# Kernel optimization log

Hardware: AMD Instinct MI355X
Metric: run time of the kernel (lower is better)

Reference implementation:

```python
import jax, jax.numpy as jnp
import numpy as np

K = 5  # kernel_size


def _unfold(x, k):
    """Torch F.unfold equivalent: [B,C,H,W] -> [B,C,k*k,H,W].
    Patch index is row-major over the kxk window (dy*k+dx), matching
    F.unfold's channel-major / window-row-major layout after view(B,C,k*k,H,W)."""
    p = k // 2
    B, C, H, W = x.shape
    xp = jnp.pad(x, ((0, 0), (0, 0), (p, p), (p, p)))
    patches = [xp[:, :, dy:dy + H, dx:dx + W] for dy in range(k) for dx in range(k)]
    return jnp.stack(patches, axis=2)


def _conv2d(x, w, b, pad):
    y = jax.lax.conv_general_dilated(
        x, w, window_strides=(1, 1), padding=[(pad, pad), (pad, pad)],
        dimension_numbers=("NCHW", "OIHW", "NCHW"))
    return y + b[None, :, None, None]


def setup_inputs() -> dict:
    key = jax.random.key(0)
    k0, k1, k2 = jax.random.split(key, 3)
    B, H, W = 2, 1024, 1024
    flow = jax.random.normal(k0, (B, 2, H, W), jnp.float32)
    # kernel_gen params: Conv2d(3,32,3,pad=1) -> ReLU -> Conv2d(32,50,1)
    w1 = jax.random.normal(k1, (32, 3, 3, 3), jnp.float32) * 0.1
    b1 = jnp.zeros((32,), jnp.float32)
    w2 = jax.random.normal(k2, (K * K * 2, 32, 1, 1), jnp.float32) * 0.1
    b2 = jnp.zeros((K * K * 2,), jnp.float32)
    return {"flow": flow, "w1": w1, "b1": b1, "w2": w2, "b2": b2}


def reference(flow, w1, b1, w2, b2):
    B, _, H, W = flow.shape
    patches = _unfold(flow, K)                       # [B,2,25,H,W]
    # torch .var(dim=2) defaults to unbiased (ddof=1)
    var = jnp.var(patches, axis=2, ddof=1)           # [B,2,H,W]
    consistency = jnp.exp(-jnp.sqrt(jnp.sum(var * var, axis=1, keepdims=True)))  # [B,1,H,W]
    guidance = jnp.concatenate([flow, consistency], axis=1)  # [B,3,H,W]
    h = jax.nn.relu(_conv2d(guidance, w1, b1, pad=1))        # [B,32,H,W]
    kernels = _conv2d(h, w2, b2, pad=0).reshape(B, 2, K * K, H, W)
    refined = jnp.sum(kernels * patches, axis=2)             # [B,2,H,W]
    return refined
```

## Files before the change

kernel.cpp:

```cpp
#include <hip/hip_runtime.h>
#include <math.h>

#define KSZ 5
#define TS 16
#define HALO 3
#define FW (TS + 2*HALO)
#define FWP (FW + 1)
#define CW (TS + 2)
#define CWP (CW + 1)
#define SF_C (FW*FWP)
#define SC_BASE (2*SF_C)

typedef __attribute__((ext_vector_type(8))) short short8_t;
typedef __attribute__((ext_vector_type(4))) float float4_t;
typedef __attribute__((ext_vector_type(2))) unsigned int uint2_t;

static __device__ __forceinline__ unsigned short f2bf(float f) {
    union { float f; unsigned int u; } v; v.f = f;
    return (unsigned short)((v.u + 0x7FFFu + ((v.u >> 16) & 1u)) >> 16);
}
static __device__ __forceinline__ unsigned int pk2t(float a, float b) {
    union { float f; unsigned int u; } ua, ub; ua.f = a; ub.f = b;
    return __builtin_amdgcn_perm(ub.u, ua.u, 0x07060302u);
}

static __device__ __forceinline__ void slot_decode(int n, int& c, int& sel, int& idx, bool& valid) {
    int g4c = (n >> 2) & 3;
    c = g4c >> 1; sel = g4c & 1;
    idx = ((n >> 4) << 2) + (n & 3);
    valid = sel ? (idx < 10) : (idx < 15);
}

__global__ __launch_bounds__(256)
void pack_kernel(const float* __restrict__ w1, const float* __restrict__ b1,
                 const float* __restrict__ w2, const float* __restrict__ b2,
                 unsigned short* __restrict__ wp, float* __restrict__ bp)
{
    const int tid = threadIdx.x;
    for (int i = tid; i < 6*64*8; i += 256) {
        int f = i >> 9, l = (i >> 3) & 63, j = i & 7;
        int m = l & 15, k = ((l >> 4) << 3) + j;
        float v;
        if (f < 2) { int row = f*16 + m; v = (k < 27) ? w1[row*27 + k] : 0.f; }
        else {
            int n = (f - 2)*16 + m;
            int c, sel, idx; bool valid;
            slot_decode(n, c, sel, idx, valid);
            int jj = sel*15 + idx;
            v = valid ? w2[(c*25 + jj)*32 + k] : 0.f;
        }
        wp[i] = f2bf(v);
    }
    for (int i = tid; i < 6*64*4; i += 256) {
        int f = i >> 8, l = (i >> 2) & 63, r = i & 3, g4 = l >> 4;
        float v;
        if (f < 2) v = b1[f*16 + g4*4 + r];
        else {
            int n = (f - 2)*16 + g4*4 + r;
            int c, sel, idx; bool valid;
            slot_decode(n, c, sel, idx, valid);
            v = valid ? b2[c*25 + sel*15 + idx] : 0.f;
        }
        bp[i] = v;
    }
}

__global__ __launch_bounds__(256)
void refine_kernel(const float* __restrict__ flow,
                   const unsigned short* __restrict__ wp,
                   const float* __restrict__ bp,
                   float* __restrict__ out, int H, int W)
{
    __shared__ float smf[SC_BASE + CW*CWP];
    __shared__ __align__(16) char dyn[6400];

    const int tid = threadIdx.x;
    const int x0 = blockIdx.x * TS;
    const int y0 = blockIdx.y * TS;
    const int b  = blockIdx.z;

    const int lane = tid & 63;
    const int wave = tid >> 6;
    const int col  = lane & 15;
    const int g4   = lane >> 4;
    const int key  = col >> 2;

    short8_t w1A[2], w2A[4];
    float4_t cb1[2], cb2[4];
    #pragma unroll
    for (int nt = 0; nt < 2; ++nt) {
        w1A[nt] = *(const short8_t*)&wp[(nt*64 + lane)*8];
        cb1[nt] = *(const float4_t*)&bp[(nt*64 + lane)*4];
    }
    #pragma unroll
    for (int nt = 0; nt < 4; ++nt) {
        w2A[nt] = *(const short8_t*)&wp[((2+nt)*64 + lane)*8];
        cb2[nt] = *(const float4_t*)&bp[((2+nt)*64 + lane)*4];
    }

    for (int c = 0; c < 2; ++c) {
        const float* src = flow + ((size_t)(b*2+c) * H) * W;
        for (int i = tid; i < FW*FW; i += 256) {
            int ly = i / FW, lx = i - ly*FW;
            int gy = y0 - HALO + ly, gx = x0 - HALO + lx;
            float v = 0.f;
            if (gy >= 0 && gy < H && gx >= 0 && gx < W) v = src[(size_t)gy*W + gx];
            smf[c*SF_C + ly*FWP + lx] = v;
        }
    }
    __syncthreads();

    {
        float4_t* rs = (float4_t*)dyn;
        for (int i = tid; i < FW*CW; i += 256) {
            int y = i / CW, x = i - y*CW;
            const float* r0 = &smf[y*FWP + x];
            const float* r1 = &smf[SF_C + y*FWP + x];
            float s0 = 0.f, q0 = 0.f, s1 = 0.f, q1 = 0.f;
            #pragma unroll
            for (int dx = 0; dx < KSZ; ++dx) {
                float a = r0[dx]; s0 += a; q0 = fmaf(a, a, q0);
                float c = r1[dx]; s1 += c; q1 = fmaf(c, c, q1);
            }
            rs[i] = (float4_t){s0, q0, s1, q1};
        }
    }
    __syncthreads();

    for (int i = tid; i < CW*CW; i += 256) {
        int py = i / CW, px = i - py*CW;
        int gy = y0 - 1 + py, gx = x0 - 1 + px;
        float cons = 0.f;
        if (gy >= 0 && gy < H && gx >= 0 && gx < W) {
            const float4_t* rp = (const float4_t*)dyn + py*CW + px;
            float4_t acc = rp[0];
            #pragma unroll
            for (int dy = 1; dy < KSZ; ++dy) acc += rp[dy*CW];
            float v0 = (acc.y - acc.x*acc.x*(1.f/25.f)) * (1.f/24.f);
            float v1 = (acc.w - acc.z*acc.z*(1.f/25.f)) * (1.f/24.f);
            cons = __expf(-sqrtf(v0*v0 + v1*v1));
        }
        smf[SC_BASE + py*CWP + px] = cons;
    }
    __syncthreads();

    unsigned short* hb = (unsigned short*)dyn;

    int goff[8], gpitch[8];
    #pragma unroll
    for (int j = 0; j < 8; ++j) {
        int ch = g4*8 + j;
        int chc = (ch < 27) ? ch : 0;
        int c = chc / 9, rem = chc - 9*c;
        int ky = rem / 3, kx = rem - 3*ky;
        if (c < 2) { goff[j] = c*SF_C + (2+ky)*FWP + (2+kx) + col; gpitch[j] = FWP; }
        else       { goff[j] = SC_BASE + ky*CWP + kx + col;        gpitch[j] = CWP; }
        goff[j] += wave*4 * gpitch[j];
    }

    const int sel = g4 & 1, pc = g4 >> 1;
    int pb = pc*SF_C + sel*(3*FWP) + FWP + 1 + col + (wave*4)*FWP;

    const int hrow = (wave*16 + col) * 64;
    const int hw0 = hrow + (((0*2 + (g4 >> 1)) ^ key) << 4) + ((g4 & 1) << 3);
    const int hw1 = hrow + (((1*2 + (g4 >> 1)) ^ key) << 4) + ((g4 & 1) << 3);
    const int hro = hrow + ((g4 ^ key) << 4);

    #pragma unroll
    for (int mt = 0; mt < 4; ++mt) {
        const int ty = wave*4 + mt;

        unsigned int gd[4];
        #pragma unroll
        for (int t = 0; t < 4; ++t)
            gd[t] = pk2t(smf[goff[2*t]], smf[goff[2*t+1]]);
        #pragma unroll
        for (int j = 0; j < 8; ++j) goff[j] += gpitch[j];
        union { unsigned int u[4]; short8_t s; } gu;
        gu.u[0] = gd[0]; gu.u[1] = gd[1]; gu.u[2] = gd[2]; gu.u[3] = gd[3];
        short8_t gB = gu.s;

        float4_t h0 = __builtin_amdgcn_mfma_f32_16x16x32_bf16(w1A[0], gB, cb1[0], 0, 0, 0);
        float4_t h1 = __builtin_amdgcn_mfma_f32_16x16x32_bf16(w1A[1], gB, cb1[1], 0, 0, 0);

        {
            uint2_t d0, d1;
            d0.x = pk2t(fmaxf(h0[0],0.f), fmaxf(h0[1],0.f));
            d0.y = pk2t(fmaxf(h0[2],0.f), fmaxf(h0[3],0.f));
            d1.x = pk2t(fmaxf(h1[0],0.f), fmaxf(h1[1],0.f));
            d1.y = pk2t(fmaxf(h1[2],0.f), fmaxf(h1[3],0.f));
            *(uint2_t*)((char*)hb + hw0) = d0;
            *(uint2_t*)((char*)hb + hw1) = d1;
        }
        short8_t hf = *(const short8_t*)((char*)hb + hro);

        float4_t ka[4];
        #pragma unroll
        for (int nt = 0; nt < 4; ++nt)
            ka[nt] = __builtin_amdgcn_mfma_f32_16x16x32_bf16(w2A[nt], hf, cb2[nt], 0, 0, 0);

        float s = 0.f;
        #pragma unroll
        for (int idx = 0; idx < 16; ++idx) {
            float pv = smf[pb + (idx/5)*FWP + (idx%5)];
            s = fmaf(ka[idx >> 2][idx & 3], pv, s);
        }
        pb += FWP;

        s += __shfl_xor(s, 16);

        if ((g4 & 1) == 0) {
            int y = y0 + ty, x = x0 + col;
            out[((size_t)(b*2 + pc) * H + y) * W + x] = s;
        }
    }
}

extern "C" void kernel_launch(void* const* d_in, const int* in_sizes, int n_in,
                              void* d_out, int out_size, void* d_ws, size_t ws_size,
                              hipStream_t stream) {
    const float* flow = (const float*)d_in[0];
    const float* w1   = (const float*)d_in[1];
    const float* b1   = (const float*)d_in[2];
    const float* w2   = (const float*)d_in[3];
    const float* b2   = (const float*)d_in[4];
    float* out = (float*)d_out;

    unsigned short* wp = (unsigned short*)d_ws;
    float* bp = (float*)((char*)d_ws + 8192);

    const int H = 1024, W = 1024;
    const int B = in_sizes[0] / (2 * H * W);

    pack_kernel<<<1, 256, 0, stream>>>(w1, b1, w2, b2, wp, bp);
    dim3 grid(W / TS, H / TS, B);
    refine_kernel<<<grid, dim3(256), 0, stream>>>(flow, wp, bp, out, H, W);
}
```

Before: 130.9 us.

## Permute conv1 K-slots for uniform LDS gathers and reuse patch rows in registers

The conv1 weight packing reorders the 27 input taps into K-slots, and the consistency map now uses the same pitch as the flow tiles. Together these let each lane gather its 8 bf16 operands from one base pointer plus constant offsets instead of 8 separately computed addresses. The 5-wide row-sum stage computes two outputs per thread with a sliding update, so fewer LDS reads are needed. In the main loop the 15 patch values are kept in registers and shifted by one row per iteration, so only 5 new LDS loads are issued each step. The cost is more register pressure and more complex index logic, and the sliding sums may round slightly differently.

```diff
diff --git a/kernel.cpp b/kernel.cpp
--- a/kernel.cpp
+++ b/kernel.cpp
@@ -7,9 +7,9 @@
 #define FW (TS + 2*HALO)
 #define FWP (FW + 1)
 #define CW (TS + 2)
-#define CWP (CW + 1)
 #define SF_C (FW*FWP)
 #define SC_BASE (2*SF_C)
+#define SMF_TOT (SC_BASE + 18*FWP)
 
 typedef __attribute__((ext_vector_type(8))) short short8_t;
 typedef __attribute__((ext_vector_type(4))) float float4_t;
@@ -29,6 +29,15 @@
     c = g4c >> 1; sel = g4c & 1;
     idx = ((n >> 4) << 2) + (n & 3);
     valid = sel ? (idx < 10) : (idx < 15);
+}
+
+static __device__ __forceinline__ int kperm(int s) {
+    int sg = s >> 3, sj = s & 7;
+    if (sg < 3) return sg*9 + sj;
+    if (sj == 1) return 8;
+    if (sj == 2) return 17;
+    if (sj == 4) return 26;
+    return -1;
 }
 
 __global__ __launch_bounds__(256)
@@ -39,15 +48,16 @@
     const int tid = threadIdx.x;
     for (int i = tid; i < 6*64*8; i += 256) {
         int f = i >> 9, l = (i >> 3) & 63, j = i & 7;
-        int m = l & 15, k = ((l >> 4) << 3) + j;
+        int m = l & 15, s = ((l >> 4) << 3) + j;
         float v;
-        if (f < 2) { int row = f*16 + m; v = (k < 27) ? w1[row*27 + k] : 0.f; }
-        else {
+        if (f < 2) {
+            int k = kperm(s);
+            v = (k >= 0) ? w1[(f*16 + m)*27 + k] : 0.f;
+        } else {
             int n = (f - 2)*16 + m;
             int c, sel, idx; bool valid;
             slot_decode(n, c, sel, idx, valid);
-            int jj = sel*15 + idx;
-            v = valid ? w2[(c*25 + jj)*32 + k] : 0.f;
+            v = valid ? w2[(c*25 + sel*15 + idx)*32 + s] : 0.f;
         }
         wp[i] = f2bf(v);
     }
@@ -71,7 +81,7 @@
                    const float* __restrict__ bp,
                    float* __restrict__ out, int H, int W)
 {
-    __shared__ float smf[SC_BASE + CW*CWP];
+    __shared__ float smf[SMF_TOT];
     __shared__ __align__(16) char dyn[6400];
 
     const int tid = threadIdx.x;
@@ -112,17 +122,22 @@
 
     {
         float4_t* rs = (float4_t*)dyn;
-        for (int i = tid; i < FW*CW; i += 256) {
-            int y = i / CW, x = i - y*CW;
-            const float* r0 = &smf[y*FWP + x];
-            const float* r1 = &smf[SF_C + y*FWP + x];
-            float s0 = 0.f, q0 = 0.f, s1 = 0.f, q1 = 0.f;
-            #pragma unroll
-            for (int dx = 0; dx < KSZ; ++dx) {
-                float a = r0[dx]; s0 += a; q0 = fmaf(a, a, q0);
-                float c = r1[dx]; s1 += c; q1 = fmaf(c, c, q1);
-            }
-            rs[i] = (float4_t){s0, q0, s1, q1};
+        if (tid < FW*(CW/2)) {
+            int y = tid / (CW/2), xp = (tid - y*(CW/2)) * 2;
+            const float* r0 = &smf[y*FWP + xp];
+            const float* r1 = &smf[SF_C + y*FWP + xp];
+            float a0=r0[0], a1=r0[1], a2=r0[2], a3=r0[3], a4=r0[4], a5=r0[5];
+            float c0=r1[0], c1=r1[1], c2=r1[2], c3=r1[3], c4=r1[4], c5=r1[5];
+            float sA = ((a0+a1)+(a2+a3))+a4;
+            float qA = fmaf(a4,a4, fmaf(a3,a3, fmaf(a2,a2, fmaf(a1,a1, a0*a0))));
+            float sB = ((c0+c1)+(c2+c3))+c4;
+            float qB = fmaf(c4,c4, fmaf(c3,c3, fmaf(c2,c2, fmaf(c1,c1, c0*c0))));
+            float sA1 = sA + a5 - a0;
+            float qA1 = fmaf(-a0, a0, fmaf(a5, a5, qA));
+            float sB1 = sB + c5 - c0;
+            float qB1 = fmaf(-c0, c0, fmaf(c5, c5, qB));
+            rs[y*CW + xp]     = (float4_t){sA,  qA,  sB,  qB };
+            rs[y*CW + xp + 1] = (float4_t){sA1, qA1, sB1, qB1};
         }
     }
     __syncthreads();
@@ -140,26 +155,29 @@
             float v1 = (acc.w - acc.z*acc.z*(1.f/25.f)) * (1.f/24.f);
             cons = __expf(-sqrtf(v0*v0 + v1*v1));
         }
-        smf[SC_BASE + py*CWP + px] = cons;
+        smf[SC_BASE + py*FWP + px] = cons;
     }
     __syncthreads();
 
     unsigned short* hb = (unsigned short*)dyn;
 
-    int goff[8], gpitch[8];
-    #pragma unroll
-    for (int j = 0; j < 8; ++j) {
-        int ch = g4*8 + j;
-        int chc = (ch < 27) ? ch : 0;
-        int c = chc / 9, rem = chc - 9*c;
-        int ky = rem / 3, kx = rem - 3*ky;
-        if (c < 2) { goff[j] = c*SF_C + (2+ky)*FWP + (2+kx) + col; gpitch[j] = FWP; }
-        else       { goff[j] = SC_BASE + ky*CWP + kx + col;        gpitch[j] = CWP; }
-        goff[j] += wave*4 * gpitch[j];
+    int gb0, gb1, gb2, gb3;
+    {
+        int ty0 = wave*4;
+        int p0 = 0*SF_C + (ty0 + 2)*FWP + (col + 2);
+        int p1 = 1*SF_C + (ty0 + 2)*FWP + (col + 2);
+        int p2 = SC_BASE + ty0*FWP + col;
+        if (g4 == 0)      { gb0 = gb1 = gb2 = gb3 = p0; }
+        else if (g4 == 1) { gb0 = gb1 = gb2 = gb3 = p1; }
+        else if (g4 == 2) { gb0 = gb1 = gb2 = gb3 = p2; }
+        else { gb0 = p0 + 47; gb1 = p1 + 46; gb2 = p2 + 24; gb3 = p0; }
     }
 
     const int sel = g4 & 1, pc = g4 >> 1;
     int pb = pc*SF_C + sel*(3*FWP) + FWP + 1 + col + (wave*4)*FWP;
+    float pv[15];
+    #pragma unroll
+    for (int i = 0; i < 15; ++i) pv[i] = smf[pb + (i/5)*FWP + (i%5)];
 
     const int hrow = (wave*16 + col) * 64;
     const int hw0 = hrow + (((0*2 + (g4 >> 1)) ^ key) << 4) + ((g4 & 1) << 3);
@@ -170,15 +188,15 @@
     for (int mt = 0; mt < 4; ++mt) {
         const int ty = wave*4 + mt;
 
-        unsigned int gd[4];
-        #pragma unroll
-        for (int t = 0; t < 4; ++t)
-            gd[t] = pk2t(smf[goff[2*t]], smf[goff[2*t+1]]);
-        #pragma unroll
-        for (int j = 0; j < 8; ++j) goff[j] += gpitch[j];
+        float ga = smf[gb0 + 0],  gbv = smf[gb0 + 1];
+        float gc = smf[gb1 + 2],  gd  = smf[gb1 + 23];
+        float ge = smf[gb2 + 24], gf  = smf[gb2 + 25];
+        float gg = smf[gb3 + 46], gh  = smf[gb3 + 47];
         union { unsigned int u[4]; short8_t s; } gu;
-        gu.u[0] = gd[0]; gu.u[1] = gd[1]; gu.u[2] = gd[2]; gu.u[3] = gd[3];
+        gu.u[0] = pk2t(ga, gbv); gu.u[1] = pk2t(gc, gd);
+        gu.u[2] = pk2t(ge, gf);  gu.u[3] = pk2t(gg, gh);
         short8_t gB = gu.s;
+        gb0 += FWP; gb1 += FWP; gb2 += FWP; gb3 += FWP;
 
         float4_t h0 = __builtin_amdgcn_mfma_f32_16x16x32_bf16(w1A[0], gB, cb1[0], 0, 0, 0);
         float4_t h1 = __builtin_amdgcn_mfma_f32_16x16x32_bf16(w1A[1], gB, cb1[1], 0, 0, 0);
@@ -201,11 +219,16 @@
 
         float s = 0.f;
         #pragma unroll
-        for (int idx = 0; idx < 16; ++idx) {
-            float pv = smf[pb + (idx/5)*FWP + (idx%5)];
-            s = fmaf(ka[idx >> 2][idx & 3], pv, s);
-        }
-        pb += FWP;
+        for (int i = 0; i < 15; ++i)
+            s = fmaf(ka[i >> 2][i & 3], pv[i], s);
+
+        if (mt < 3) {
+            #pragma unroll
+            for (int i = 0; i < 10; ++i) pv[i] = pv[i + 5];
+            pb += FWP;
+            #pragma unroll
+            for (int i = 10; i < 15; ++i) pv[i] = smf[pb + (i/5)*FWP + (i%5)];
+        }
 
         s += __shfl_xor(s, 16);
 
```

After: 126.1 us. -3.7%, faster.
